# Performance work log

Hardware: AMD Instinct MI355X
Metric: run time of the kernel (lower is better)

Reference implementation:

```python
import jax, jax.numpy as jnp
import numpy as np

EMBED_DIM = 1024
NUM_HEADS = 16
RANK = 32
HEAD_DIM = EMBED_DIM // NUM_HEADS
SCALE = 1.0 / np.sqrt(RANK).astype(np.float32)


def setup_inputs() -> dict:
    key = jax.random.key(0)
    ks = jax.random.split(key, 9)
    B, S = 2, 2048
    def lin(k, fan_in, fan_out):
        bound = 1.0 / np.sqrt(fan_in)
        return jax.random.uniform(k, (fan_in, fan_out), jnp.float32, -bound, bound)
    return {
        "hidden_states": jax.random.normal(ks[0], (B, S, EMBED_DIM), jnp.float32),
        "Wq": lin(ks[1], EMBED_DIM, RANK * NUM_HEADS),
        "bq": jnp.zeros((RANK * NUM_HEADS,), jnp.float32),
        "Wk": lin(ks[2], EMBED_DIM, RANK * NUM_HEADS),
        "bk": jnp.zeros((RANK * NUM_HEADS,), jnp.float32),
        "Wv": lin(ks[3], EMBED_DIM, EMBED_DIM),
        "bv": jnp.zeros((EMBED_DIM,), jnp.float32),
        "Wo": lin(ks[4], EMBED_DIM, EMBED_DIM),
        "bo": jnp.zeros((EMBED_DIM,), jnp.float32),
    }


def reference(hidden_states, Wq, bq, Wk, bk, Wv, bv, Wo, bo):
    B, S, E = hidden_states.shape
    q = (hidden_states @ Wq + bq).reshape(B, S, NUM_HEADS, RANK)      # [b,i,h,r]
    k = (hidden_states @ Wk + bk).reshape(B, S, NUM_HEADS, RANK)      # [b,j,h,r]
    v = (hidden_states @ Wv + bv).reshape(B, S, NUM_HEADS, HEAD_DIM)  # [b,j,h,d]
    # full [b,i,j,h] score tensor, softmax over j (axis=2), as in the torch code
    scores = jnp.einsum('bihr,bjhr->bijh', q, k) * SCALE
    attn = jax.nn.softmax(scores, axis=2)
    out = jnp.einsum('bijh,bjhd->bihd', attn, v).reshape(B, S, E)
    return out @ Wo + bo
```

## Files before the change

### kernel.cpp

```cpp
#include <hip/hip_runtime.h>

#define EMBED   1024
#define NHEADS  16
#define RANK    32
#define HDIM    64
#define BATCH   2
#define SEQ     2048
#define BSQ     (BATCH * SEQ)
#define CEXP    0.25505998f

typedef __attribute__((ext_vector_type(8))) short bf16x8;
typedef __attribute__((ext_vector_type(4))) float f32x4;

__device__ __forceinline__ float bf2f(unsigned short u) {
    union { unsigned int i; float f; } x; x.i = ((unsigned int)u) << 16;
    return x.f;
}
__device__ __forceinline__ unsigned short f2bf(float f) {
    union { float f; unsigned int i; } x; x.f = f;
    unsigned int r = x.i + 0x7FFFu + ((x.i >> 16) & 1u);
    return (unsigned short)(r >> 16);
}

#define ASYNC16(gp, lp) \
    __builtin_amdgcn_global_load_lds( \
        (const __attribute__((address_space(1))) void*)(gp), \
        (__attribute__((address_space(3))) void*)(lp), 16, 0, 0)

__global__ __launch_bounds__(256) void prep_all(
    const float* __restrict__ hs,
    const float* __restrict__ Wq, const float* __restrict__ Wk,
    const float* __restrict__ Wv, const float* __restrict__ Wo,
    const float* __restrict__ bq, const float* __restrict__ bk,
    const float* __restrict__ bv,
    unsigned short* __restrict__ hsb, unsigned short* __restrict__ wT_all,
    unsigned short* __restrict__ woT, float* __restrict__ ball)
{
    __shared__ float L[64][65];
    const int blk = blockIdx.x;
    const int t = threadIdx.x;

    if (blk < 2048) {
        const size_t i = ((size_t)blk * 256 + t) * 8;
        float4 v0 = *(const float4*)(hs + i);
        float4 v1 = *(const float4*)(hs + i + 4);
        ushort4 o0, o1;
        o0.x = f2bf(v0.x); o0.y = f2bf(v0.y); o0.z = f2bf(v0.z); o0.w = f2bf(v0.w);
        o1.x = f2bf(v1.x); o1.y = f2bf(v1.y); o1.z = f2bf(v1.z); o1.w = f2bf(v1.w);
        *(ushort4*)(hsb + i) = o0;
        *(ushort4*)(hsb + i + 4) = o1;
        return;
    }
    if (blk < 2816) {
        int idx = blk - 2048;
        int z, bx, by;
        if (idx < 256) { z = idx >> 7; int r2 = idx & 127; bx = r2 & 7; by = r2 >> 3; }
        else { idx -= 256; z = 2 + (idx >> 8); int r2 = idx & 255; bx = r2 & 15; by = r2 >> 4; }
        const int Nw = (z < 2) ? 512 : 1024;
        const float* W = (z == 0) ? Wq : (z == 1) ? Wk : (z == 2) ? Wv : Wo;
        unsigned short* dst = (z == 3) ? woT : (wT_all + (size_t)z * 512 * 1024);

        const int r = t >> 2, c0 = (t & 3) * 16;
        const float* src = W + (size_t)(by * 64 + r) * Nw + bx * 64 + c0;
        #pragma unroll
        for (int u = 0; u < 4; u++)
            *(float4*)&L[r][c0 + 4 * u] = *(const float4*)(src + 4 * u);
        __syncthreads();
        unsigned short* drow = dst + (size_t)(bx * 64 + r) * 1024 + by * 64 + c0;
        #pragma unroll
        for (int u4 = 0; u4 < 4; u4++) {
            ushort4 o;
            o.x = f2bf(L[c0 + 4 * u4 + 0][r]);
            o.y = f2bf(L[c0 + 4 * u4 + 1][r]);
            o.z = f2bf(L[c0 + 4 * u4 + 2][r]);
            o.w = f2bf(L[c0 + 4 * u4 + 3][r]);
            *(ushort4*)(drow + 4 * u4) = o;
        }
        return;
    }
    {
        const int i = (blk - 2816) * 256 + t;
        ball[i] = (i < 512) ? bq[i] : (i < 1024) ? bk[i - 512] : bv[i - 1024];
    }
}

__global__ __launch_bounds__(256) void gemm_qkv(
    const unsigned short* __restrict__ A, const unsigned short* __restrict__ BT,
    const float* __restrict__ bias,
    unsigned short* __restrict__ qH, unsigned short* __restrict__ kH,
    unsigned short* __restrict__ vTout)
{
    __shared__ unsigned short As[128 * 32];
    __shared__ unsigned short Bs[128 * 32];
    const int K = 1024;
    const int t = threadIdx.x;
    const int lane = t & 63;
    const int li = lane & 15, la = lane >> 4;
    const int w = t >> 6, wm = w >> 1, wn = w & 1;
    const int row0 = blockIdx.y * 128, col0 = blockIdx.x * 128;

    const int sr = lane >> 2, sc2 = (lane & 3) * 8;
    const unsigned short* ag0 = A + (size_t)(row0 + w * 32 + sr) * K + sc2;
    const unsigned short* ag1 = A + (size_t)(row0 + w * 32 + 16 + sr) * K + sc2;
    const unsigned short* bg0 = BT + (size_t)(col0 + w * 32 + sr) * K + sc2;
    const unsigned short* bg1 = BT + (size_t)(col0 + w * 32 + 16 + sr) * K + sc2;
    unsigned short* lA0 = &As[(w * 32) * 32];
    unsigned short* lA1 = &As[(w * 32 + 16) * 32];
    unsigned short* lB0 = &Bs[(w * 32) * 32];
    unsigned short* lB1 = &Bs[(w * 32 + 16) * 32];

    f32x4 acc[4][4];
    #pragma unroll
    for (int i = 0; i < 4; i++)
        #pragma unroll
        for (int j = 0; j < 4; j++)
            acc[i][j] = (f32x4){0.f, 0.f, 0.f, 0.f};

    for (int k0 = 0; k0 < K; k0 += 32) {
        ASYNC16(ag0 + k0, lA0);
        ASYNC16(ag1 + k0, lA1);
        ASYNC16(bg0 + k0, lB0);
        ASYNC16(bg1 + k0, lB1);
        __syncthreads();
        bf16x8 af[4], bfr[4];
        #pragma unroll
        for (int mt = 0; mt < 4; mt++)
            af[mt] = *(const bf16x8*)&As[(wm * 64 + mt * 16 + li) * 32 + la * 8];
        #pragma unroll
        for (int nt = 0; nt < 4; nt++)
            bfr[nt] = *(const bf16x8*)&Bs[(wn * 64 + nt * 16 + li) * 32 + la * 8];
        #pragma unroll
        for (int mt = 0; mt < 4; mt++)
            #pragma unroll
            for (int nt = 0; nt < 4; nt++)
                acc[mt][nt] = __builtin_amdgcn_mfma_f32_16x16x32_bf16(af[mt], bfr[nt], acc[mt][nt], 0, 0, 0);
        __syncthreads();
    }

    const int bb = row0 >> 11;
    const int jb = (row0 & 2047) + wm * 64;
    #pragma unroll
    for (int nt = 0; nt < 4; nt++) {
        const int col = col0 + wn * 64 + nt * 16 + li;
        const float bval = bias[col];
        if (col < 1024) {
            const int hh = (col & 511) >> 5;
            const int rr = col & 31;
            unsigned short* base = ((col < 512) ? qH : kH)
                + ((size_t)(bb * 16 + hh) * 2048) * 32 + rr;
            #pragma unroll
            for (int mt = 0; mt < 4; mt++)
                #pragma unroll
                for (int r = 0; r < 4; r++)
                    base[(size_t)(jb + mt * 16 + la * 4 + r) * 32] =
                        f2bf(acc[mt][nt][r] + bval);
        } else {
            const int hd = col - 1024;
            unsigned short* dcol = vTout + ((size_t)(bb * 16 + (hd >> 6)) * 64 + (hd & 63)) * SEQ;
            #pragma unroll
            for (int mt = 0; mt < 4; mt++) {
                const int srow = jb + mt * 16 + la * 4;
                ushort4 o;
                o.x = f2bf(acc[mt][nt][0] + bval);
                o.y = f2bf(acc[mt][nt][1] + bval);
                o.z = f2bf(acc[mt][nt][2] + bval);
                o.w = f2bf(acc[mt][nt][3] + bval);
                *(ushort4*)(dcol + srow) = o;
            }
        }
    }
}

__global__ __launch_bounds__(256) void gemm_out(
    const unsigned short* __restrict__ A, const unsigned short* __restrict__ BT,
    const float* __restrict__ bias, float* __restrict__ C)
{
    __shared__ unsigned short As[64 * 32];
    __shared__ unsigned short Bs[128 * 32];
    const int K = 1024;
    const int t = threadIdx.x;
    const int lane = t & 63;
    const int li = lane & 15, la = lane >> 4;
    const int w = t >> 6, wm = w >> 1, wn = w & 1;
    const int row0 = blockIdx.y * 64, col0 = blockIdx.x * 128;

    const int sr = lane >> 2, sc2 = (lane & 3) * 8;
    const unsigned short* ag0 = A + (size_t)(row0 + w * 16 + sr) * K + sc2;
    const unsigned short* bg0 = BT + (size_t)(col0 + w * 32 + sr) * K + sc2;
    const unsigned short* bg1 = BT + (size_t)(col0 + w * 32 + 16 + sr) * K + sc2;
    unsigned short* lA0 = &As[(w * 16) * 32];
    unsigned short* lB0 = &Bs[(w * 32) * 32];
    unsigned short* lB1 = &Bs[(w * 32 + 16) * 32];

    f32x4 acc[2][4];
    #pragma unroll
    for (int i = 0; i < 2; i++)
        #pragma unroll
        for (int j = 0; j < 4; j++)
            acc[i][j] = (f32x4){0.f, 0.f, 0.f, 0.f};

    for (int k0 = 0; k0 < K; k0 += 32) {
        ASYNC16(ag0 + k0, lA0);
        ASYNC16(bg0 + k0, lB0);
        ASYNC16(bg1 + k0, lB1);
        __syncthreads();
        bf16x8 af[2], bfr[4];
        #pragma unroll
        for (int mt = 0; mt < 2; mt++)
            af[mt] = *(const bf16x8*)&As[(wm * 32 + mt * 16 + li) * 32 + la * 8];
        #pragma unroll
        for (int nt = 0; nt < 4; nt++)
            bfr[nt] = *(const bf16x8*)&Bs[(wn * 64 + nt * 16 + li) * 32 + la * 8];
        #pragma unroll
        for (int mt = 0; mt < 2; mt++)
            #pragma unroll
            for (int nt = 0; nt < 4; nt++)
                acc[mt][nt] = __builtin_amdgcn_mfma_f32_16x16x32_bf16(af[mt], bfr[nt], acc[mt][nt], 0, 0, 0);
        __syncthreads();
    }

    #pragma unroll
    for (int nt = 0; nt < 4; nt++) {
        const int col = col0 + wn * 64 + nt * 16 + li;
        const float bval = bias[col];
        #pragma unroll
        for (int mt = 0; mt < 2; mt++)
            #pragma unroll
            for (int r = 0; r < 4; r++) {
                const int row = row0 + wm * 32 + mt * 16 + la * 4 + r;
                C[(size_t)row * 1024 + col] = acc[mt][nt][r] + bval;
            }
    }
}

__global__ __launch_bounds__(256, 3) void attn_v5(
    const unsigned short* __restrict__ qH,
    const unsigned short* __restrict__ kH,
    const unsigned short* __restrict__ vT,
    unsigned short* __restrict__ ao)
{
    __shared__ float smem[2688];
    unsigned short* P = (unsigned short*)smem;
    float* lbuf = smem + 2560;

    const int t = threadIdx.x;
    const int lane = t & 63;
    const int li = lane & 15, la = lane >> 4;
    const int w = t >> 6;

    const int bh = blockIdx.x & 31;
    const int itile = blockIdx.x >> 5;
    const int i0 = itile * 32;
    const int b = bh >> 4, h = bh & 15;

    bf16x8 qf[2];
    #pragma unroll
    for (int it = 0; it < 2; it++) {
        const unsigned short* qp = qH + ((size_t)bh * 2048 + i0 + it * 16 + li) * 32 + la * 8;
        ushort4 q0 = *(const ushort4*)qp;
        ushort4 q1 = *(const ushort4*)(qp + 4);
        short u[8];
        u[0] = (short)f2bf(bf2f(q0.x) * CEXP);
        u[1] = (short)f2bf(bf2f(q0.y) * CEXP);
        u[2] = (short)f2bf(bf2f(q0.z) * CEXP);
        u[3] = (short)f2bf(bf2f(q0.w) * CEXP);
        u[4] = (short)f2bf(bf2f(q1.x) * CEXP);
        u[5] = (short)f2bf(bf2f(q1.y) * CEXP);
        u[6] = (short)f2bf(bf2f(q1.z) * CEXP);
        u[7] = (short)f2bf(bf2f(q1.w) * CEXP);
        qf[it] = *(const bf16x8*)u;
    }

    bf16x8 vones;
    #pragma unroll
    for (int u2 = 0; u2 < 8; u2++) vones[u2] = (short)0x3F80;

    const unsigned short* kbase = kH + (size_t)bh * 2048 * 32
                                  + (size_t)(w * 32 + li) * 32 + la * 8;
    const unsigned short* vbase = vT + (size_t)bh * 64 * SEQ
                                  + (size_t)li * SEQ + w * 32 + la * 8;

    unsigned short* Pw = P + w * 32 * 40;

    f32x4 accO[2][4], accl[2];
    #pragma unroll
    for (int mt = 0; mt < 2; mt++) {
        accl[mt] = (f32x4){0.f, 0.f, 0.f, 0.f};
        #pragma unroll
        for (int dt = 0; dt < 4; dt++) accO[mt][dt] = (f32x4){0.f, 0.f, 0.f, 0.f};
    }

    bf16x8 kf0 = *(const bf16x8*)(kbase);
    bf16x8 kf1 = *(const bf16x8*)(kbase + 512);

    for (int j0 = 0; j0 < SEQ; j0 += 128) {
        bf16x8 vf[4];
        #pragma unroll
        for (int dt = 0; dt < 4; dt++)
            vf[dt] = *(const bf16x8*)(vbase + (size_t)dt * 16 * SEQ + j0);
        const int jn = (j0 + 128) & 2047;
        const bf16x8 kn0 = *(const bf16x8*)(kbase + (size_t)jn * 32);
        const bf16x8 kn1 = *(const bf16x8*)(kbase + (size_t)jn * 32 + 512);

        f32x4 sc[2][2];
        sc[0][0] = __builtin_amdgcn_mfma_f32_16x16x32_bf16(kf0, qf[0], (f32x4){0.f,0.f,0.f,0.f}, 0, 0, 0);
        sc[0][1] = __builtin_amdgcn_mfma_f32_16x16x32_bf16(kf0, qf[1], (f32x4){0.f,0.f,0.f,0.f}, 0, 0, 0);
        sc[1][0] = __builtin_amdgcn_mfma_f32_16x16x32_bf16(kf1, qf[0], (f32x4){0.f,0.f,0.f,0.f}, 0, 0, 0);
        sc[1][1] = __builtin_amdgcn_mfma_f32_16x16x32_bf16(kf1, qf[1], (f32x4){0.f,0.f,0.f,0.f}, 0, 0, 0);

        #pragma unroll
        for (int jt = 0; jt < 2; jt++)
            #pragma unroll
            for (int it = 0; it < 2; it++) {
                union { float f; unsigned int u; } c0, c1, c2, c3;
                c0.f = exp2f(sc[jt][it][0]);
                c1.f = exp2f(sc[jt][it][1]);
                c2.f = exp2f(sc[jt][it][2]);
                c3.f = exp2f(sc[jt][it][3]);
                uint2 pk;
                pk.x = __builtin_amdgcn_perm(c1.u + 0x8000u, c0.u + 0x8000u, 0x07060302u);
                pk.y = __builtin_amdgcn_perm(c3.u + 0x8000u, c2.u + 0x8000u, 0x07060302u);
                *(uint2*)&Pw[(it * 16 + li) * 40 + jt * 16 + la * 4] = pk;
            }

        #pragma unroll
        for (int mt = 0; mt < 2; mt++) {
            const bf16x8 af = *(const bf16x8*)&Pw[(mt * 16 + li) * 40 + la * 8];
            accl[mt] = __builtin_amdgcn_mfma_f32_16x16x32_bf16(af, vones, accl[mt], 0, 0, 0);
            #pragma unroll
            for (int dt = 0; dt < 4; dt++)
                accO[mt][dt] = __builtin_amdgcn_mfma_f32_16x16x32_bf16(af, vf[dt], accO[mt][dt], 0, 0, 0);
        }
        kf0 = kn0; kf1 = kn1;
    }

    if (li == 0) {
        #pragma unroll
        for (int mt = 0; mt < 2; mt++) {
            float4 tv;
            tv.x = accl[mt][0]; tv.y = accl[mt][1];
            tv.z = accl[mt][2]; tv.w = accl[mt][3];
            *(float4*)&lbuf[w * 32 + mt * 16 + la * 4] = tv;
        }
    }
    __syncthreads();

    const int ir = w * 8 + (lane >> 3);
    const int dl = (lane & 7) * 2;
    const float lsum = lbuf[ir] + lbuf[32 + ir] + lbuf[64 + ir] + lbuf[96 + ir];
    const float linv = 1.0f / lsum;
    float* obuf = smem;
    unsigned short* aorow = ao + ((size_t)(b * SEQ + i0 + ir)) * 1024 + h * 64 + dl;

    #pragma unroll
    for (int s = 0; s < 4; s++) {
        float* ow = obuf + w * 512;
        #pragma unroll
        for (int mt = 0; mt < 2; mt++)
            #pragma unroll
            for (int r = 0; r < 4; r++)
                ow[(mt * 16 + la * 4 + r) * 16 + li] = accO[mt][s][r];
        __syncthreads();
        float v0 = 0.f, v1 = 0.f;
        #pragma unroll
        for (int w2 = 0; w2 < 4; w2++) {
            const float2 x = *(const float2*)&obuf[w2 * 512 + ir * 16 + dl];
            v0 += x.x; v1 += x.y;
        }
        const unsigned int outp = (unsigned int)f2bf(v0 * linv)
                                | ((unsigned int)f2bf(v1 * linv) << 16);
        *(unsigned int*)(aorow + s * 16) = outp;
        __syncthreads();
    }
}

extern "C" void kernel_launch(void* const* d_in, const int* in_sizes, int n_in,
                              void* d_out, int out_size, void* d_ws, size_t ws_size,
                              hipStream_t stream) {
    const float* hs = (const float*)d_in[0];
    const float* Wq = (const float*)d_in[1];
    const float* bq = (const float*)d_in[2];
    const float* Wk = (const float*)d_in[3];
    const float* bk = (const float*)d_in[4];
    const float* Wv = (const float*)d_in[5];
    const float* bv = (const float*)d_in[6];
    const float* Wo = (const float*)d_in[7];
    const float* bo = (const float*)d_in[8];

    char* p = (char*)d_ws;
    unsigned short* hsb = (unsigned short*)(p);
    unsigned short* wT  = (unsigned short*)(p + 8388608u);
    unsigned short* woT = (unsigned short*)(p + 12582912u);
    float*          ball= (float*)(p + 14680064u);
    unsigned short* qHb = (unsigned short*)(p + 14688256u);
    unsigned short* kHb = (unsigned short*)(p + 18882560u);
    unsigned short* vTb = (unsigned short*)(p + 23076864u);
    unsigned short* ao  = (unsigned short*)(p + 31465472u);

    prep_all<<<dim3(2824), 256, 0, stream>>>(hs, Wq, Wk, Wv, Wo, bq, bk, bv,
                                             hsb, wT, woT, ball);

    gemm_qkv<<<dim3(16, 32), 256, 0, stream>>>(hsb, wT, ball, qHb, kHb, vTb);

    attn_v5<<<dim3(2048), 256, 0, stream>>>(qHb, kHb, vTb, ao);

    gemm_out<<<dim3(8, 64), 256, 0, stream>>>(ao, woT, bo, (float*)d_out);
}
```

Measured before the change: 211.9 us.

## Share K/V tiles across waves in LDS with 128-row query blocks

The attention kernel now gives each block 128 query rows (32 per wave) and all 64 KV rows per step. K and V tiles are staged cooperatively into shared memory with a register prefetch, instead of each wave splitting the key range and reading global memory directly. Because each wave owns full rows, the cross-wave reduction of partial outputs and row sums through shared memory is removed and results are written directly. In exchange there are two barriers per KV step, more LDS reads, only 512 blocks, and output stores become scattered 2-byte writes.

```diff
diff --git a/kernel.cpp b/kernel.cpp
--- a/kernel.cpp
+++ b/kernel.cpp
@@ -233,15 +233,15 @@
     }
 }
 
-__global__ __launch_bounds__(256, 3) void attn_v5(
+__global__ __launch_bounds__(256) void attn_v6(
     const unsigned short* __restrict__ qH,
     const unsigned short* __restrict__ kH,
     const unsigned short* __restrict__ vT,
     unsigned short* __restrict__ ao)
 {
-    __shared__ float smem[2688];
-    unsigned short* P = (unsigned short*)smem;
-    float* lbuf = smem + 2560;
+    __shared__ unsigned short kt[64 * 48];
+    __shared__ unsigned short vt[64 * 72];
+    __shared__ unsigned short P[128 * 72];
 
     const int t = threadIdx.x;
     const int lane = t & 63;
@@ -250,13 +250,13 @@
 
     const int bh = blockIdx.x & 31;
     const int itile = blockIdx.x >> 5;
-    const int i0 = itile * 32;
+    const int i0 = itile * 128;
     const int b = bh >> 4, h = bh & 15;
 
     bf16x8 qf[2];
     #pragma unroll
     for (int it = 0; it < 2; it++) {
-        const unsigned short* qp = qH + ((size_t)bh * 2048 + i0 + it * 16 + li) * 32 + la * 8;
+        const unsigned short* qp = qH + ((size_t)bh * 2048 + i0 + w * 32 + it * 16 + li) * 32 + la * 8;
         ushort4 q0 = *(const ushort4*)qp;
         ushort4 q1 = *(const ushort4*)(qp + 4);
         short u[8];
@@ -275,12 +275,11 @@
     #pragma unroll
     for (int u2 = 0; u2 < 8; u2++) vones[u2] = (short)0x3F80;
 
-    const unsigned short* kbase = kH + (size_t)bh * 2048 * 32
-                                  + (size_t)(w * 32 + li) * 32 + la * 8;
-    const unsigned short* vbase = vT + (size_t)bh * 64 * SEQ
-                                  + (size_t)li * SEQ + w * 32 + la * 8;
-
-    unsigned short* Pw = P + w * 32 * 40;
+    const unsigned short* kbase = kH + (size_t)bh * 2048 * 32;
+    const unsigned short* vbase = vT + (size_t)bh * 64 * SEQ;
+
+    const int kr = t >> 2, kc = (t & 3) * 8;
+    const int vr = t >> 3, vc = (t & 7) * 8;
 
     f32x4 accO[2][4], accl[2];
     #pragma unroll
@@ -290,26 +289,32 @@
         for (int dt = 0; dt < 4; dt++) accO[mt][dt] = (f32x4){0.f, 0.f, 0.f, 0.f};
     }
 
-    bf16x8 kf0 = *(const bf16x8*)(kbase);
-    bf16x8 kf1 = *(const bf16x8*)(kbase + 512);
-
-    for (int j0 = 0; j0 < SEQ; j0 += 128) {
-        bf16x8 vf[4];
-        #pragma unroll
-        for (int dt = 0; dt < 4; dt++)
-            vf[dt] = *(const bf16x8*)(vbase + (size_t)dt * 16 * SEQ + j0);
-        const int jn = (j0 + 128) & 2047;
-        const bf16x8 kn0 = *(const bf16x8*)(kbase + (size_t)jn * 32);
-        const bf16x8 kn1 = *(const bf16x8*)(kbase + (size_t)jn * 32 + 512);
-
-        f32x4 sc[2][2];
-        sc[0][0] = __builtin_amdgcn_mfma_f32_16x16x32_bf16(kf0, qf[0], (f32x4){0.f,0.f,0.f,0.f}, 0, 0, 0);
-        sc[0][1] = __builtin_amdgcn_mfma_f32_16x16x32_bf16(kf0, qf[1], (f32x4){0.f,0.f,0.f,0.f}, 0, 0, 0);
-        sc[1][0] = __builtin_amdgcn_mfma_f32_16x16x32_bf16(kf1, qf[0], (f32x4){0.f,0.f,0.f,0.f}, 0, 0, 0);
-        sc[1][1] = __builtin_amdgcn_mfma_f32_16x16x32_bf16(kf1, qf[1], (f32x4){0.f,0.f,0.f,0.f}, 0, 0, 0);
-
-        #pragma unroll
-        for (int jt = 0; jt < 2; jt++)
+    uint4 kreg  = *(const uint4*)(kbase + (size_t)kr * 32 + kc);
+    uint4 vreg0 = *(const uint4*)(vbase + (size_t)vr * SEQ + vc);
+    uint4 vreg1 = *(const uint4*)(vbase + (size_t)(vr + 32) * SEQ + vc);
+
+    for (int j0 = 0; j0 < SEQ; j0 += 64) {
+        __syncthreads();
+        *(uint4*)&kt[kr * 48 + kc] = kreg;
+        *(uint4*)&vt[vr * 72 + vc] = vreg0;
+        *(uint4*)&vt[(vr + 32) * 72 + vc] = vreg1;
+        __syncthreads();
+
+        const int jn = (j0 + 64) & 2047;
+        kreg  = *(const uint4*)(kbase + (size_t)(jn + kr) * 32 + kc);
+        vreg0 = *(const uint4*)(vbase + (size_t)vr * SEQ + jn + vc);
+        vreg1 = *(const uint4*)(vbase + (size_t)(vr + 32) * SEQ + jn + vc);
+
+        f32x4 sc[4][2];
+        #pragma unroll
+        for (int jt = 0; jt < 4; jt++) {
+            const bf16x8 kf = *(const bf16x8*)&kt[(jt * 16 + li) * 48 + la * 8];
+            sc[jt][0] = __builtin_amdgcn_mfma_f32_16x16x32_bf16(kf, qf[0], (f32x4){0.f,0.f,0.f,0.f}, 0, 0, 0);
+            sc[jt][1] = __builtin_amdgcn_mfma_f32_16x16x32_bf16(kf, qf[1], (f32x4){0.f,0.f,0.f,0.f}, 0, 0, 0);
+        }
+
+        #pragma unroll
+        for (int jt = 0; jt < 4; jt++)
             #pragma unroll
             for (int it = 0; it < 2; it++) {
                 union { float f; unsigned int u; } c0, c1, c2, c3;
@@ -320,57 +325,36 @@
                 uint2 pk;
                 pk.x = __builtin_amdgcn_perm(c1.u + 0x8000u, c0.u + 0x8000u, 0x07060302u);
                 pk.y = __builtin_amdgcn_perm(c3.u + 0x8000u, c2.u + 0x8000u, 0x07060302u);
-                *(uint2*)&Pw[(it * 16 + li) * 40 + jt * 16 + la * 4] = pk;
+                *(uint2*)&P[(w * 32 + it * 16 + li) * 72 + jt * 16 + la * 4] = pk;
             }
 
         #pragma unroll
         for (int mt = 0; mt < 2; mt++) {
-            const bf16x8 af = *(const bf16x8*)&Pw[(mt * 16 + li) * 40 + la * 8];
-            accl[mt] = __builtin_amdgcn_mfma_f32_16x16x32_bf16(af, vones, accl[mt], 0, 0, 0);
-            #pragma unroll
-            for (int dt = 0; dt < 4; dt++)
-                accO[mt][dt] = __builtin_amdgcn_mfma_f32_16x16x32_bf16(af, vf[dt], accO[mt][dt], 0, 0, 0);
+            #pragma unroll
+            for (int ks = 0; ks < 2; ks++) {
+                const bf16x8 pf = *(const bf16x8*)&P[(w * 32 + mt * 16 + li) * 72 + ks * 32 + la * 8];
+                accl[mt] = __builtin_amdgcn_mfma_f32_16x16x32_bf16(pf, vones, accl[mt], 0, 0, 0);
+                #pragma unroll
+                for (int dt = 0; dt < 4; dt++) {
+                    const bf16x8 vf = *(const bf16x8*)&vt[(dt * 16 + li) * 72 + ks * 32 + la * 8];
+                    accO[mt][dt] = __builtin_amdgcn_mfma_f32_16x16x32_bf16(pf, vf, accO[mt][dt], 0, 0, 0);
+                }
+            }
         }
-        kf0 = kn0; kf1 = kn1;
-    }
-
-    if (li == 0) {
-        #pragma unroll
-        for (int mt = 0; mt < 2; mt++) {
-            float4 tv;
-            tv.x = accl[mt][0]; tv.y = accl[mt][1];
-            tv.z = accl[mt][2]; tv.w = accl[mt][3];
-            *(float4*)&lbuf[w * 32 + mt * 16 + la * 4] = tv;
-        }
-    }
-    __syncthreads();
-
-    const int ir = w * 8 + (lane >> 3);
-    const int dl = (lane & 7) * 2;
-    const float lsum = lbuf[ir] + lbuf[32 + ir] + lbuf[64 + ir] + lbuf[96 + ir];
-    const float linv = 1.0f / lsum;
-    float* obuf = smem;
-    unsigned short* aorow = ao + ((size_t)(b * SEQ + i0 + ir)) * 1024 + h * 64 + dl;
-
-    #pragma unroll
-    for (int s = 0; s < 4; s++) {
-        float* ow = obuf + w * 512;
-        #pragma unroll
-        for (int mt = 0; mt < 2; mt++)
-            #pragma unroll
-            for (int r = 0; r < 4; r++)
-                ow[(mt * 16 + la * 4 + r) * 16 + li] = accO[mt][s][r];
-        __syncthreads();
-        float v0 = 0.f, v1 = 0.f;
-        #pragma unroll
-        for (int w2 = 0; w2 < 4; w2++) {
-            const float2 x = *(const float2*)&obuf[w2 * 512 + ir * 16 + dl];
-            v0 += x.x; v1 += x.y;
-        }
-        const unsigned int outp = (unsigned int)f2bf(v0 * linv)
-                                | ((unsigned int)f2bf(v1 * linv) << 16);
-        *(unsigned int*)(aorow + s * 16) = outp;
-        __syncthreads();
+    }
+
+    #pragma unroll
+    for (int mt = 0; mt < 2; mt++) {
+        float linv[4];
+        #pragma unroll
+        for (int r = 0; r < 4; r++) linv[r] = 1.f / accl[mt][r];
+        #pragma unroll
+        for (int dt = 0; dt < 4; dt++)
+            #pragma unroll
+            for (int r = 0; r < 4; r++) {
+                const int row = b * SEQ + i0 + w * 32 + mt * 16 + la * 4 + r;
+                ao[(size_t)row * 1024 + h * 64 + dt * 16 + li] = f2bf(accO[mt][dt][r] * linv[r]);
+            }
     }
 }
 
@@ -402,7 +386,7 @@
 
     gemm_qkv<<<dim3(16, 32), 256, 0, stream>>>(hsb, wT, ball, qHb, kHb, vTb);
 
-    attn_v5<<<dim3(2048), 256, 0, stream>>>(qHb, kHb, vTb, ao);
+    attn_v6<<<dim3(512), 256, 0, stream>>>(qHb, kHb, vTb, ao);
 
     gemm_out<<<dim3(8, 64), 256, 0, stream>>>(ao, woT, bo, (float*)d_out);
 }
```

New measurement: 198.6 us. 6.3% less time.
